# Optimization experiments

Measured on AMD Instinct MI355X. Metric: run time of the kernel, lower is better.

The kernel has to match this reference:

```python
import math
import jax, jax.numpy as jnp
import numpy as np

N = 8192
IN_DIM = 512
INTER = 512
HID = 1024
OUT = 512
GROUPS = 16
EPS = 1e-5


def setup_inputs() -> dict:
    key = jax.random.key(0)
    ks = jax.random.split(key, 12)
    w = lambda k, shape: jax.random.normal(k, shape, jnp.float32) * 0.02
    return {
        "h": jax.random.normal(ks[0], (N, IN_DIM), jnp.float32),
        "D": jax.random.uniform(ks[1], (N, N), dtype=jnp.float32),
        "h_prime": jax.random.normal(ks[2], (N, OUT), jnp.float32),
        "Wq": w(ks[3], (INTER, IN_DIM)), "bq": jnp.zeros((INTER,), jnp.float32),
        "Wk": w(ks[4], (INTER, IN_DIM)), "bk": jnp.zeros((INTER,), jnp.float32),
        "Wv": w(ks[5], (INTER, IN_DIM)), "bv": jnp.zeros((INTER,), jnp.float32),
        "Wr": w(ks[6], (HID, INTER)), "br": jnp.zeros((HID,), jnp.float32),
        "Wc": w(ks[7], (HID, OUT)), "bc": jnp.zeros((HID,), jnp.float32),
        "Wp": w(ks[8], (OUT, 2 * HID)), "bp": jnp.zeros((OUT,), jnp.float32),
        "alpha": jnp.full((OUT,), 0.25, jnp.float32),       # PReLU per-channel slope
        "gamma": jnp.ones((OUT,), jnp.float32),             # GroupNorm weight
        "beta": jnp.zeros((OUT,), jnp.float32),             # GroupNorm bias
    }


def reference(h, D, h_prime, Wq, bq, Wk, bk, Wv, bv, Wr, br, Wc, bc, Wp, bp, alpha, gamma, beta):
    Q = h @ Wq.T + bq                                    # [N, inter]
    K = h @ Wk.T + bk
    V = h @ Wv.T + bv
    scores = (Q @ K.T) / math.sqrt(INTER)                # [N, N]
    attn = jax.nn.softmax(D * scores, axis=-1)           # decay-masked softmax
    h_ret = attn @ V                                     # [N, inter]
    h_ret = jax.nn.gelu(h_ret @ Wr.T + br, approximate=False)  # torch GELU (erf)
    h_cat = h_prime @ Wc.T + bc                          # [N, hid]
    x = jnp.concatenate([h_ret, h_cat], axis=-1) @ Wp.T + bp   # [N, out]
    x = jnp.where(x >= 0, x, alpha * x)                  # PReLU, per-channel
    # GroupNorm over [1, out, N]: stats per group over (channels_in_group, N)
    xT = x.T                                             # [out, N]
    grp = xT.reshape(GROUPS, (OUT // GROUPS) * N)
    mean = grp.mean(axis=1, keepdims=True)
    var = grp.var(axis=1, keepdims=True)
    grp = (grp - mean) * jax.lax.rsqrt(var + EPS)
    xT = grp.reshape(OUT, N) * gamma[:, None] + beta[:, None]
    return xT.T                                          # [N, out]
```

## Files before the change

kernel.cpp:

```cpp
#include <hip/hip_runtime.h>
#include <stdint.h>
#include <math.h>

typedef float f32x4 __attribute__((ext_vector_type(4)));
typedef __bf16 bf16x8 __attribute__((ext_vector_type(8)));
typedef unsigned int u32x4 __attribute__((ext_vector_type(4)));
typedef unsigned short u16;

#define DEVINL static __device__ __forceinline__

DEVINL u16 f2bf(float f) {
  union { float f; unsigned u; } x; x.f = f;
  unsigned r = x.u + 0x7fffu + ((x.u >> 16) & 1u);
  return (u16)(r >> 16);
}

DEVINL void gload_lds16(const void* g, void* l) {
  __builtin_amdgcn_global_load_lds(
      (__attribute__((address_space(1))) void*)(g),
      (__attribute__((address_space(3))) void*)(l), 16, 0, 0);
}

__global__ void cast_kernel(const float* __restrict__ src, u16* __restrict__ dst, int n) {
  int i = (blockIdx.x * 256 + threadIdx.x) * 4;
  if (i >= n) return;
  float4 v = *(const float4*)(src + i);
  u16 o[4] = { f2bf(v.x), f2bf(v.y), f2bf(v.z), f2bf(v.w) };
  *(uint64_t*)(dst + i) = *(uint64_t*)o;
}

template<int EPI>
__global__ __launch_bounds__(256, 2) void gemm_nt(
    const u16* __restrict__ A, int lda, const u16* __restrict__ B, int ldb,
    void* __restrict__ C, int ldc, int coff,
    const float* __restrict__ bias, const float* __restrict__ alpha,
    int N128, int K, float scale)
{
  __shared__ __align__(16) u16 at[2][128 * 64];
  __shared__ __align__(16) u16 bt[2][128 * 64];
  const int tid = threadIdx.x;
  const int w = tid >> 6, lane = tid & 63, r = lane & 15, kg = lane >> 4;
  const int bm = blockIdx.x / N128, bn = blockIdx.x % N128;
  const int m0 = bm * 128, n0 = bn * 128;

  f32x4 acc[4][4];
  #pragma unroll
  for (int m = 0; m < 4; ++m)
    #pragma unroll
    for (int n = 0; n < 4; ++n) acc[m][n] = f32x4{0.f, 0.f, 0.f, 0.f};

  const int srow = tid >> 3, sc = tid & 7;
  const int nk = K >> 6;

  #pragma unroll
  for (int i = 0; i < 4; ++i) {
    int row = srow + i * 32, cs = (sc ^ row) & 7;
    gload_lds16(A + (size_t)(m0 + row) * lda + cs * 8, at[0] + i * 2048 + w * 512);
    gload_lds16(B + (size_t)(n0 + row) * ldb + cs * 8, bt[0] + i * 2048 + w * 512);
  }
  __syncthreads();

  for (int kt = 0; kt < nk; ++kt) {
    const int cur = kt & 1;
    if (kt + 1 < nk) {
      #pragma unroll
      for (int i = 0; i < 4; ++i) {
        int row = srow + i * 32, cs = (sc ^ row) & 7;
        int kcol = (kt + 1) * 64 + cs * 8;
        gload_lds16(A + (size_t)(m0 + row) * lda + kcol, at[cur ^ 1] + i * 2048 + w * 512);
        gload_lds16(B + (size_t)(n0 + row) * ldb + kcol, bt[cur ^ 1] + i * 2048 + w * 512);
      }
    }
    #pragma unroll
    for (int ks = 0; ks < 2; ++ks) {
      bf16x8 af[4], bff[4];
      #pragma unroll
      for (int m = 0; m < 4; ++m) {
        int row = (w >> 1) * 64 + m * 16 + r;
        int cs = ((ks * 4 + kg) ^ row) & 7;
        af[m] = *(const bf16x8*)(at[cur] + row * 64 + cs * 8);
      }
      #pragma unroll
      for (int n = 0; n < 4; ++n) {
        int row = (w & 1) * 64 + n * 16 + r;
        int cs = ((ks * 4 + kg) ^ row) & 7;
        bff[n] = *(const bf16x8*)(bt[cur] + row * 64 + cs * 8);
      }
      #pragma unroll
      for (int m = 0; m < 4; ++m)
        #pragma unroll
        for (int n = 0; n < 4; ++n)
          acc[m][n] = __builtin_amdgcn_mfma_f32_16x16x32_bf16(af[m], bff[n], acc[m][n], 0, 0, 0);
    }
    __syncthreads();
  }

  #pragma unroll
  for (int m = 0; m < 4; ++m) {
    #pragma unroll
    for (int n = 0; n < 4; ++n) {
      const int gcol = n0 + (w & 1) * 64 + n * 16 + r;
      #pragma unroll
      for (int reg = 0; reg < 4; ++reg) {
        const int grow = m0 + (w >> 1) * 64 + m * 16 + kg * 4 + reg;
        float v = acc[m][n][reg];
        if (EPI == 0) v = (v + bias[gcol]) * scale;
        if (EPI == 1) v = v + bias[grow];
        if (EPI == 2) { v += bias[gcol]; v = 0.5f * v * (1.f + erff(v * 0.70710678118654752f)); }
        if (EPI == 3) {
          v += bias[gcol];
          float a = alpha[gcol];
          v = (v >= 0.f) ? v : a * v;
          ((float*)C)[(size_t)grow * ldc + coff + gcol] = v;
        } else {
          ((u16*)C)[(size_t)grow * ldc + coff + gcol] = f2bf(v);
        }
      }
    }
  }
}

__global__ __launch_bounds__(256, 2) void sgemm_exp(
    const u16* __restrict__ A, const u16* __restrict__ B,
    u16* __restrict__ P, const float* __restrict__ Dmat, float* __restrict__ psum)
{
  __shared__ __align__(16) u16 at[2][128 * 64];
  __shared__ __align__(16) u16 bt[2][128 * 64];
  const int tid = threadIdx.x;
  const int w = tid >> 6, lane = tid & 63, r = lane & 15, kg = lane >> 4;
  const int xcd = blockIdx.x & 7, i = blockIdx.x >> 3;
  const int bm = (xcd >> 1) * 16 + (i & 15);
  const int bn = (xcd & 1) * 32 + (i >> 4);
  const int m0 = bm * 128, n0 = bn * 128;

  f32x4 acc[4][4];
  #pragma unroll
  for (int m = 0; m < 4; ++m)
    #pragma unroll
    for (int n = 0; n < 4; ++n) acc[m][n] = f32x4{0.f, 0.f, 0.f, 0.f};
  float dreg[64];

  const int srow = tid >> 3, sc = tid & 7;
  const int gcolb = n0 + (w & 1) * 64 + r;
  const int growb = m0 + (w >> 1) * 64 + kg * 4;

  #pragma unroll
  for (int ii = 0; ii < 4; ++ii) {
    int row = srow + ii * 32, cs = (sc ^ row) & 7;
    gload_lds16(A + (size_t)(m0 + row) * 512 + cs * 8, at[0] + ii * 2048 + w * 512);
    gload_lds16(B + (size_t)(n0 + row) * 512 + cs * 8, bt[0] + ii * 2048 + w * 512);
  }
  __syncthreads();

  #pragma unroll
  for (int kt = 0; kt < 8; ++kt) {
    const int cur = kt & 1;
    if (kt < 7) {
      #pragma unroll
      for (int ii = 0; ii < 4; ++ii) {
        int row = srow + ii * 32, cs = (sc ^ row) & 7;
        int kcol = (kt + 1) * 64 + cs * 8;
        gload_lds16(A + (size_t)(m0 + row) * 512 + kcol, at[cur ^ 1] + ii * 2048 + w * 512);
        gload_lds16(B + (size_t)(n0 + row) * 512 + kcol, bt[cur ^ 1] + ii * 2048 + w * 512);
      }
    }
    #pragma unroll
    for (int q = 0; q < 8; ++q) {
      const int id = kt * 8 + q;
      const int m = id >> 4, n = (id >> 2) & 3, reg = id & 3;
      dreg[id] = __builtin_nontemporal_load(
          Dmat + (size_t)(growb + m * 16 + reg) * 8192 + (gcolb + n * 16));
    }
    #pragma unroll
    for (int ks = 0; ks < 2; ++ks) {
      bf16x8 af[4], bff[4];
      #pragma unroll
      for (int m = 0; m < 4; ++m) {
        int row = (w >> 1) * 64 + m * 16 + r;
        int cs = ((ks * 4 + kg) ^ row) & 7;
        af[m] = *(const bf16x8*)(at[cur] + row * 64 + cs * 8);
      }
      #pragma unroll
      for (int n = 0; n < 4; ++n) {
        int row = (w & 1) * 64 + n * 16 + r;
        int cs = ((ks * 4 + kg) ^ row) & 7;
        bff[n] = *(const bf16x8*)(bt[cur] + row * 64 + cs * 8);
      }
      #pragma unroll
      for (int m = 0; m < 4; ++m)
        #pragma unroll
        for (int n = 0; n < 4; ++n)
          acc[m][n] = __builtin_amdgcn_mfma_f32_16x16x32_bf16(af[m], bff[n], acc[m][n], 0, 0, 0);
    }
    __syncthreads();
  }

  #pragma unroll
  for (int m = 0; m < 4; ++m) {
    float rs[4] = {0.f, 0.f, 0.f, 0.f};
    #pragma unroll
    for (int n = 0; n < 4; ++n) {
      const int gcol = gcolb + n * 16;
      #pragma unroll
      for (int reg = 0; reg < 4; ++reg) {
        const int grow = growb + m * 16 + reg;
        const float p = __expf(acc[m][n][reg] * dreg[m * 16 + n * 4 + reg]);
        rs[reg] += p;
        P[(size_t)grow * 8192 + gcol] = f2bf(p);
      }
    }
    #pragma unroll
    for (int reg = 0; reg < 4; ++reg) {
      float v = rs[reg];
      v += __shfl_xor(v, 1); v += __shfl_xor(v, 2);
      v += __shfl_xor(v, 4); v += __shfl_xor(v, 8);
      if (r == 0)
        psum[(size_t)(growb + m * 16 + reg) * 128 + bn * 2 + (w & 1)] = v;
    }
  }
}

__global__ __launch_bounds__(256, 2) void pv_split(
    const u16* __restrict__ P, const u16* __restrict__ VT, float* __restrict__ Opart)
{
  __shared__ __align__(16) u16 at[2][128 * 64];
  __shared__ __align__(16) u16 bt[2][128 * 64];
  const int tid = threadIdx.x;
  const int w = tid >> 6, lane = tid & 63, r = lane & 15, kg = lane >> 4;
  const int xcd = blockIdx.x & 7, i = blockIdx.x >> 3;
  const int bn = i & 3, ks = (i >> 2) & 3, bm = xcd * 8 + (i >> 4);
  const int m0 = bm * 128, n0 = bn * 128;
  const int koff = ks * 2048;

  f32x4 acc[4][4];
  #pragma unroll
  for (int m = 0; m < 4; ++m)
    #pragma unroll
    for (int n = 0; n < 4; ++n) acc[m][n] = f32x4{0.f, 0.f, 0.f, 0.f};

  const int srow = tid >> 3, sc = tid & 7;

  #pragma unroll
  for (int ii = 0; ii < 4; ++ii) {
    int row = srow + ii * 32, cs = (sc ^ row) & 7;
    gload_lds16(P  + (size_t)(m0 + row) * 8192 + koff + cs * 8, at[0] + ii * 2048 + w * 512);
    gload_lds16(VT + (size_t)(n0 + row) * 8192 + koff + cs * 8, bt[0] + ii * 2048 + w * 512);
  }
  __syncthreads();

  for (int kt = 0; kt < 32; ++kt) {
    const int cur = kt & 1;
    if (kt < 31) {
      #pragma unroll
      for (int ii = 0; ii < 4; ++ii) {
        int row = srow + ii * 32, cs = (sc ^ row) & 7;
        int kcol = koff + (kt + 1) * 64 + cs * 8;
        gload_lds16(P  + (size_t)(m0 + row) * 8192 + kcol, at[cur ^ 1] + ii * 2048 + w * 512);
        gload_lds16(VT + (size_t)(n0 + row) * 8192 + kcol, bt[cur ^ 1] + ii * 2048 + w * 512);
      }
    }
    #pragma unroll
    for (int ks2 = 0; ks2 < 2; ++ks2) {
      bf16x8 af[4], bff[4];
      #pragma unroll
      for (int m = 0; m < 4; ++m) {
        int row = (w >> 1) * 64 + m * 16 + r;
        int cs = ((ks2 * 4 + kg) ^ row) & 7;
        af[m] = *(const bf16x8*)(at[cur] + row * 64 + cs * 8);
      }
      #pragma unroll
      for (int n = 0; n < 4; ++n) {
        int row = (w & 1) * 64 + n * 16 + r;
        int cs = ((ks2 * 4 + kg) ^ row) & 7;
        bff[n] = *(const bf16x8*)(bt[cur] + row * 64 + cs * 8);
      }
      #pragma unroll
      for (int m = 0; m < 4; ++m)
        #pragma unroll
        for (int n = 0; n < 4; ++n)
          acc[m][n] = __builtin_amdgcn_mfma_f32_16x16x32_bf16(af[m], bff[n], acc[m][n], 0, 0, 0);
    }
    __syncthreads();
  }

  float* op = Opart + (size_t)ks * 4194304;
  #pragma unroll
  for (int m = 0; m < 4; ++m) {
    #pragma unroll
    for (int n = 0; n < 4; ++n) {
      const int gcol = n0 + (w & 1) * 64 + n * 16 + r;
      #pragma unroll
      for (int reg = 0; reg < 4; ++reg) {
        const int grow = m0 + (w >> 1) * 64 + m * 16 + kg * 4 + reg;
        __builtin_nontemporal_store(acc[m][n][reg], op + (size_t)grow * 512 + gcol);
      }
    }
  }
}

__global__ __launch_bounds__(256) void pv_combine(
    const float* __restrict__ Opart, const float* __restrict__ ls, u16* __restrict__ hrb)
{
  const int idx = (blockIdx.x * 256 + threadIdx.x) * 4;
  const int row = idx >> 9;
  const float li = 1.f / ls[row];
  float4 a = *(const float4*)(Opart + idx);
  const float4 b = *(const float4*)(Opart + 4194304 + idx);
  const float4 c = *(const float4*)(Opart + 8388608 + idx);
  const float4 d = *(const float4*)(Opart + 12582912 + idx);
  a.x = (a.x + b.x + c.x + d.x) * li;
  a.y = (a.y + b.y + c.y + d.y) * li;
  a.z = (a.z + b.z + c.z + d.z) * li;
  a.w = (a.w + b.w + c.w + d.w) * li;
  u16 o[4] = { f2bf(a.x), f2bf(a.y), f2bf(a.z), f2bf(a.w) };
  *(uint64_t*)(hrb + idx) = *(uint64_t*)o;
}

__global__ __launch_bounds__(256) void rowsum_kernel(const float* __restrict__ psum,
                                                     float* __restrict__ ls) {
  const int row = blockIdx.x * 4 + (threadIdx.x >> 6);
  const int lane = threadIdx.x & 63;
  const float2 v = *(const float2*)(psum + (size_t)row * 128 + lane * 2);
  float s = v.x + v.y;
  #pragma unroll
  for (int m = 1; m < 64; m <<= 1) s += __shfl_xor(s, m);
  if (lane == 0) ls[row] = s;
}

__global__ void gn_stats_kernel(const float* __restrict__ x, float* __restrict__ part) {
  const int g = blockIdx.x >> 4, ch = blockIdx.x & 15;
  const int t = threadIdx.x;
  float s = 0.f, ss = 0.f;
  const int cl = (t & 7) * 4;
  const int r0 = ch * 512 + (t >> 3);
  for (int i = 0; i < 16; ++i) {
    const float4 v = *(const float4*)(x + (size_t)(r0 + i * 32) * 512 + g * 32 + cl);
    s += v.x + v.y + v.z + v.w;
    ss += v.x * v.x + v.y * v.y + v.z * v.z + v.w * v.w;
  }
  #pragma unroll
  for (int m = 1; m < 64; m <<= 1) { s += __shfl_xor(s, m); ss += __shfl_xor(ss, m); }
  __shared__ float red[8];
  const int w = t >> 6, lane = t & 63;
  if (lane == 0) { red[w * 2] = s; red[w * 2 + 1] = ss; }
  __syncthreads();
  if (t == 0) {
    part[blockIdx.x * 2]     = red[0] + red[2] + red[4] + red[6];
    part[blockIdx.x * 2 + 1] = red[1] + red[3] + red[5] + red[7];
  }
}

__global__ void gn_finalize_kernel(const float* __restrict__ part, float* __restrict__ mv) {
  const int g = threadIdx.x;
  if (g < 16) {
    float s = 0.f, ss = 0.f;
    for (int ch = 0; ch < 16; ++ch) {
      s  += part[(g * 16 + ch) * 2];
      ss += part[(g * 16 + ch) * 2 + 1];
    }
    const float mean = s * (1.f / 262144.f);
    const float var = ss * (1.f / 262144.f) - mean * mean;
    mv[g * 2] = mean;
    mv[g * 2 + 1] = rsqrtf(var + 1e-5f);
  }
}

__global__ void gn_norm_kernel(const float* __restrict__ x, const float* __restrict__ mv,
                               const float* __restrict__ gamma, const float* __restrict__ beta,
                               float* __restrict__ out) {
  const int idx = (blockIdx.x * 256 + threadIdx.x) * 4;
  const int c = idx & 511, g = c >> 5;
  const float mean = mv[g * 2], rs = mv[g * 2 + 1];
  float4 v = *(const float4*)(x + idx);
  const float4 gm = *(const float4*)(gamma + c);
  const float4 bt = *(const float4*)(beta + c);
  v.x = (v.x - mean) * rs * gm.x + bt.x;
  v.y = (v.y - mean) * rs * gm.y + bt.y;
  v.z = (v.z - mean) * rs * gm.z + bt.z;
  v.w = (v.w - mean) * rs * gm.w + bt.w;
  *(float4*)(out + idx) = v;
}

extern "C" void kernel_launch(void* const* d_in, const int* in_sizes, int n_in,
                              void* d_out, int out_size, void* d_ws, size_t ws_size,
                              hipStream_t stream) {
  (void)in_sizes; (void)n_in; (void)out_size; (void)ws_size;
  const float* h     = (const float*)d_in[0];
  const float* Dm    = (const float*)d_in[1];
  const float* hp    = (const float*)d_in[2];
  const float* Wq    = (const float*)d_in[3];
  const float* bq    = (const float*)d_in[4];
  const float* Wk    = (const float*)d_in[5];
  const float* bk    = (const float*)d_in[6];
  const float* Wv    = (const float*)d_in[7];
  const float* bv    = (const float*)d_in[8];
  const float* Wr    = (const float*)d_in[9];
  const float* br    = (const float*)d_in[10];
  const float* Wc    = (const float*)d_in[11];
  const float* bc    = (const float*)d_in[12];
  const float* Wp    = (const float*)d_in[13];
  const float* bp    = (const float*)d_in[14];
  const float* alpha = (const float*)d_in[15];
  const float* gamma = (const float*)d_in[16];
  const float* beta  = (const float*)d_in[17];

  char* ws = (char*)d_ws;
  const size_t MB = 1ull << 20;
  u16*   P    = (u16*)(ws);
  u16*   hb   = (u16*)(ws);
  u16*   xcat = (u16*)(ws);
  float* xf   = (float*)(ws + 32 * MB);
  u16*   hpb  = (u16*)(ws + 128 * MB);
  u16*   Qb   = (u16*)(ws + 144 * MB);
  u16*   hrb  = (u16*)(ws + 144 * MB);
  u16*   Kb   = (u16*)(ws + 152 * MB);
  u16*   VTb  = (u16*)(ws + 160 * MB);
  u16*   Wqb  = (u16*)(ws + 168 * MB);
  u16*   Wkb  = Wqb + 262144;
  u16*   Wvb  = Wkb + 262144;
  u16*   Wrb  = Wvb + 262144;
  u16*   Wcb  = Wrb + 524288;
  u16*   Wpb  = Wcb + 524288;
  float* lsum = (float*)(ws + 168 * MB + 5767168);
  float* gp   = lsum + 8192;
  float* mv   = gp + 512;
  float* psum = (float*)(ws + 176 * MB);
  float* Opart = (float*)(ws + 184 * MB);

  cast_kernel<<<4096, 256, 0, stream>>>(h, hb, 4194304);
  cast_kernel<<<4096, 256, 0, stream>>>(hp, hpb, 4194304);
  cast_kernel<<<256, 256, 0, stream>>>(Wq, Wqb, 262144);
  cast_kernel<<<256, 256, 0, stream>>>(Wk, Wkb, 262144);
  cast_kernel<<<256, 256, 0, stream>>>(Wv, Wvb, 262144);
  cast_kernel<<<512, 256, 0, stream>>>(Wr, Wrb, 524288);
  cast_kernel<<<512, 256, 0, stream>>>(Wc, Wcb, 524288);
  cast_kernel<<<1024, 256, 0, stream>>>(Wp, Wpb, 1048576);

  gemm_nt<0><<<256, 256, 0, stream>>>(hb, 512, Wqb, 512, Qb, 512, 0, bq, nullptr, 4, 512, 0.044194173824159216f);
  gemm_nt<0><<<256, 256, 0, stream>>>(hb, 512, Wkb, 512, Kb, 512, 0, bk, nullptr, 4, 512, 1.0f);
  gemm_nt<1><<<256, 256, 0, stream>>>(Wvb, 512, hb, 512, VTb, 8192, 0, bv, nullptr, 64, 512, 1.0f);

  sgemm_exp<<<4096, 256, 0, stream>>>(Qb, Kb, P, Dm, psum);
  rowsum_kernel<<<2048, 256, 0, stream>>>(psum, lsum);

  pv_split<<<1024, 256, 0, stream>>>(P, VTb, Opart);
  pv_combine<<<4096, 256, 0, stream>>>(Opart, lsum, hrb);

  gemm_nt<2><<<512, 256, 0, stream>>>(hrb, 512, Wrb, 512, xcat, 2048, 0, br, nullptr, 8, 512, 1.0f);
  gemm_nt<0><<<512, 256, 0, stream>>>(hpb, 512, Wcb, 512, xcat, 2048, 1024, bc, nullptr, 8, 512, 1.0f);

  gemm_nt<3><<<256, 256, 0, stream>>>(xcat, 2048, Wpb, 2048, xf, 512, 0, bp, alpha, 4, 2048, 1.0f);

  gn_stats_kernel<<<256, 256, 0, stream>>>(xf, gp);
  gn_finalize_kernel<<<1, 64, 0, stream>>>(gp, mv);
  gn_norm_kernel<<<4096, 256, 0, stream>>>(xf, mv, gamma, beta, (float*)d_out);
}
```

Baseline: 423.6 us.

## Halve K-tile to 32 in QK and PV GEMMs to raise occupancy

Shrinks the LDS K-tile in the score+exp GEMM and the split-K PV GEMM from 64 to 32 columns, with a new swizzled staging layout that packs two rows per 128-byte line. LDS per block drops by half, and launch bounds are raised to 3 and 4 blocks per CU to hide memory latency. The cost is twice as many barriers and prefetch iterations per tile, less MFMA work between syncs, and tighter register budgets that may cause spills, especially with the 64 D-matrix registers in sgemm_exp.

```diff
diff --git a/kernel.cpp b/kernel.cpp
--- a/kernel.cpp
+++ b/kernel.cpp
@@ -19,6 +19,23 @@
   __builtin_amdgcn_global_load_lds(
       (__attribute__((address_space(1))) void*)(g),
       (__attribute__((address_space(3))) void*)(l), 16, 0, 0);
+}
+
+DEVINL void stage32(const u16* __restrict__ src0, size_t lda, u16* lds, int w, int lane) {
+  #pragma unroll
+  for (int h = 0; h < 2; ++h) {
+    const int idx = h * 256 + w * 64 + lane;
+    const int line = idx >> 3, slot = idx & 7;
+    const int u = slot ^ (line & 7);
+    const int row = line * 2 + (u >> 2), c4 = u & 3;
+    gload_lds16(src0 + (size_t)row * lda + c4 * 8, lds + h * 2048 + w * 512);
+  }
+}
+
+DEVINL bf16x8 ldfrag(const u16* buf, int row, int kg) {
+  const int line = row >> 1;
+  const int slot = (((row & 1) * 4 + kg) ^ (line & 7));
+  return *(const bf16x8*)((const char*)buf + line * 128 + slot * 16);
 }
 
 __global__ void cast_kernel(const float* __restrict__ src, u16* __restrict__ dst, int n) {
@@ -120,12 +137,12 @@
   }
 }
 
-__global__ __launch_bounds__(256, 2) void sgemm_exp(
+__global__ __launch_bounds__(256, 3) void sgemm_exp(
     const u16* __restrict__ A, const u16* __restrict__ B,
     u16* __restrict__ P, const float* __restrict__ Dmat, float* __restrict__ psum)
 {
-  __shared__ __align__(16) u16 at[2][128 * 64];
-  __shared__ __align__(16) u16 bt[2][128 * 64];
+  __shared__ __align__(16) u16 abuf[2][128 * 32];
+  __shared__ __align__(16) u16 bbuf[2][128 * 32];
   const int tid = threadIdx.x;
   const int w = tid >> 6, lane = tid & 63, r = lane & 15, kg = lane >> 4;
   const int xcd = blockIdx.x & 7, i = blockIdx.x >> 3;
@@ -140,58 +157,37 @@
     for (int n = 0; n < 4; ++n) acc[m][n] = f32x4{0.f, 0.f, 0.f, 0.f};
   float dreg[64];
 
-  const int srow = tid >> 3, sc = tid & 7;
   const int gcolb = n0 + (w & 1) * 64 + r;
   const int growb = m0 + (w >> 1) * 64 + kg * 4;
 
-  #pragma unroll
-  for (int ii = 0; ii < 4; ++ii) {
-    int row = srow + ii * 32, cs = (sc ^ row) & 7;
-    gload_lds16(A + (size_t)(m0 + row) * 512 + cs * 8, at[0] + ii * 2048 + w * 512);
-    gload_lds16(B + (size_t)(n0 + row) * 512 + cs * 8, bt[0] + ii * 2048 + w * 512);
-  }
+  stage32(A + (size_t)m0 * 512, 512, abuf[0], w, lane);
+  stage32(B + (size_t)n0 * 512, 512, bbuf[0], w, lane);
   __syncthreads();
 
   #pragma unroll
-  for (int kt = 0; kt < 8; ++kt) {
+  for (int kt = 0; kt < 16; ++kt) {
     const int cur = kt & 1;
-    if (kt < 7) {
-      #pragma unroll
-      for (int ii = 0; ii < 4; ++ii) {
-        int row = srow + ii * 32, cs = (sc ^ row) & 7;
-        int kcol = (kt + 1) * 64 + cs * 8;
-        gload_lds16(A + (size_t)(m0 + row) * 512 + kcol, at[cur ^ 1] + ii * 2048 + w * 512);
-        gload_lds16(B + (size_t)(n0 + row) * 512 + kcol, bt[cur ^ 1] + ii * 2048 + w * 512);
-      }
-    }
-    #pragma unroll
-    for (int q = 0; q < 8; ++q) {
-      const int id = kt * 8 + q;
+    if (kt < 15) {
+      stage32(A + (size_t)m0 * 512 + (kt + 1) * 32, 512, abuf[cur ^ 1], w, lane);
+      stage32(B + (size_t)n0 * 512 + (kt + 1) * 32, 512, bbuf[cur ^ 1], w, lane);
+    }
+    #pragma unroll
+    for (int q = 0; q < 4; ++q) {
+      const int id = kt * 4 + q;
       const int m = id >> 4, n = (id >> 2) & 3, reg = id & 3;
       dreg[id] = __builtin_nontemporal_load(
           Dmat + (size_t)(growb + m * 16 + reg) * 8192 + (gcolb + n * 16));
     }
-    #pragma unroll
-    for (int ks = 0; ks < 2; ++ks) {
-      bf16x8 af[4], bff[4];
-      #pragma unroll
-      for (int m = 0; m < 4; ++m) {
-        int row = (w >> 1) * 64 + m * 16 + r;
-        int cs = ((ks * 4 + kg) ^ row) & 7;
-        af[m] = *(const bf16x8*)(at[cur] + row * 64 + cs * 8);
-      }
-      #pragma unroll
-      for (int n = 0; n < 4; ++n) {
-        int row = (w & 1) * 64 + n * 16 + r;
-        int cs = ((ks * 4 + kg) ^ row) & 7;
-        bff[n] = *(const bf16x8*)(bt[cur] + row * 64 + cs * 8);
-      }
-      #pragma unroll
-      for (int m = 0; m < 4; ++m)
-        #pragma unroll
-        for (int n = 0; n < 4; ++n)
-          acc[m][n] = __builtin_amdgcn_mfma_f32_16x16x32_bf16(af[m], bff[n], acc[m][n], 0, 0, 0);
-    }
+    bf16x8 af[4], bff[4];
+    #pragma unroll
+    for (int m = 0; m < 4; ++m) af[m] = ldfrag(abuf[cur], (w >> 1) * 64 + m * 16 + r, kg);
+    #pragma unroll
+    for (int n = 0; n < 4; ++n) bff[n] = ldfrag(bbuf[cur], (w & 1) * 64 + n * 16 + r, kg);
+    #pragma unroll
+    for (int m = 0; m < 4; ++m)
+      #pragma unroll
+      for (int n = 0; n < 4; ++n)
+        acc[m][n] = __builtin_amdgcn_mfma_f32_16x16x32_bf16(af[m], bff[n], acc[m][n], 0, 0, 0);
     __syncthreads();
   }
 
@@ -220,11 +216,11 @@
   }
 }
 
-__global__ __launch_bounds__(256, 2) void pv_split(
+__global__ __launch_bounds__(256, 4) void pv_split(
     const u16* __restrict__ P, const u16* __restrict__ VT, float* __restrict__ Opart)
 {
-  __shared__ __align__(16) u16 at[2][128 * 64];
-  __shared__ __align__(16) u16 bt[2][128 * 64];
+  __shared__ __align__(16) u16 abuf[2][128 * 32];
+  __shared__ __align__(16) u16 bbuf[2][128 * 32];
   const int tid = threadIdx.x;
   const int w = tid >> 6, lane = tid & 63, r = lane & 15, kg = lane >> 4;
   const int xcd = blockIdx.x & 7, i = blockIdx.x >> 3;
@@ -238,48 +234,29 @@
     #pragma unroll
     for (int n = 0; n < 4; ++n) acc[m][n] = f32x4{0.f, 0.f, 0.f, 0.f};
 
-  const int srow = tid >> 3, sc = tid & 7;
-
-  #pragma unroll
-  for (int ii = 0; ii < 4; ++ii) {
-    int row = srow + ii * 32, cs = (sc ^ row) & 7;
-    gload_lds16(P  + (size_t)(m0 + row) * 8192 + koff + cs * 8, at[0] + ii * 2048 + w * 512);
-    gload_lds16(VT + (size_t)(n0 + row) * 8192 + koff + cs * 8, bt[0] + ii * 2048 + w * 512);
-  }
+  const u16* Pa  = P  + (size_t)m0 * 8192 + koff;
+  const u16* Vb  = VT + (size_t)n0 * 8192 + koff;
+
+  stage32(Pa, 8192, abuf[0], w, lane);
+  stage32(Vb, 8192, bbuf[0], w, lane);
   __syncthreads();
 
-  for (int kt = 0; kt < 32; ++kt) {
+  for (int kt = 0; kt < 64; ++kt) {
     const int cur = kt & 1;
-    if (kt < 31) {
-      #pragma unroll
-      for (int ii = 0; ii < 4; ++ii) {
-        int row = srow + ii * 32, cs = (sc ^ row) & 7;
-        int kcol = koff + (kt + 1) * 64 + cs * 8;
-        gload_lds16(P  + (size_t)(m0 + row) * 8192 + kcol, at[cur ^ 1] + ii * 2048 + w * 512);
-        gload_lds16(VT + (size_t)(n0 + row) * 8192 + kcol, bt[cur ^ 1] + ii * 2048 + w * 512);
-      }
-    }
-    #pragma unroll
-    for (int ks2 = 0; ks2 < 2; ++ks2) {
-      bf16x8 af[4], bff[4];
-      #pragma unroll
-      for (int m = 0; m < 4; ++m) {
-        int row = (w >> 1) * 64 + m * 16 + r;
-        int cs = ((ks2 * 4 + kg) ^ row) & 7;
-        af[m] = *(const bf16x8*)(at[cur] + row * 64 + cs * 8);
-      }
-      #pragma unroll
-      for (int n = 0; n < 4; ++n) {
-        int row = (w & 1) * 64 + n * 16 + r;
-        int cs = ((ks2 * 4 + kg) ^ row) & 7;
-        bff[n] = *(const bf16x8*)(bt[cur] + row * 64 + cs * 8);
-      }
-      #pragma unroll
-      for (int m = 0; m < 4; ++m)
-        #pragma unroll
-        for (int n = 0; n < 4; ++n)
-          acc[m][n] = __builtin_amdgcn_mfma_f32_16x16x32_bf16(af[m], bff[n], acc[m][n], 0, 0, 0);
-    }
+    if (kt < 63) {
+      stage32(Pa + (kt + 1) * 32, 8192, abuf[cur ^ 1], w, lane);
+      stage32(Vb + (kt + 1) * 32, 8192, bbuf[cur ^ 1], w, lane);
+    }
+    bf16x8 af[4], bff[4];
+    #pragma unroll
+    for (int m = 0; m < 4; ++m) af[m] = ldfrag(abuf[cur], (w >> 1) * 64 + m * 16 + r, kg);
+    #pragma unroll
+    for (int n = 0; n < 4; ++n) bff[n] = ldfrag(bbuf[cur], (w & 1) * 64 + n * 16 + r, kg);
+    #pragma unroll
+    for (int m = 0; m < 4; ++m)
+      #pragma unroll
+      for (int n = 0; n < 4; ++n)
+        acc[m][n] = __builtin_amdgcn_mfma_f32_16x16x32_bf16(af[m], bff[n], acc[m][n], 0, 0, 0);
     __syncthreads();
   }
 
```

Result: slower. 648.9 us (+53.2%).
